# Kernel optimization log

Hardware: AMD Instinct MI355X
Metric: run time of the kernel (lower is better)

The kernel has to match this reference:

```python
import jax, jax.numpy as jnp
import numpy as np

E, D, H, T = 64, 512, 1024, 256  # num_experts, dim, hidden_dim, tokens


def setup_inputs() -> dict:
    key = jax.random.key(0)
    k1, k2, k3, k4 = jax.random.split(key, 4)
    x = jax.random.normal(k1, (T, D), dtype=jnp.float32)
    expert_idx = jax.random.randint(k2, (T,), 0, E, dtype=jnp.int64)
    # kaiming_uniform-ish init scale for the batched expert weights
    fc1_w = jax.random.normal(k3, (E, H, D), dtype=jnp.float32) * 0.02  # [E, hidden, dim]
    fc2_w = jax.random.normal(k4, (E, D, H), dtype=jnp.float32) * 0.02  # [E, dim, hidden]
    return {"x": x, "expert_idx": expert_idx, "fc1_w": fc1_w, "fc2_w": fc2_w}


def reference(x, expert_idx, fc1_w, fc2_w):
    # Gather full expert weight matrices per token (faithful to torch module),
    # then per-token matvec: out = silu(x @ W1^T) @ W2^T
    w1 = fc1_w[expert_idx]                      # [T, H, D]
    w2 = fc2_w[expert_idx]                      # [T, D, H]
    h = jax.nn.silu(jnp.einsum('td,thd->th', x, w1))  # [T, H]
    out = jnp.einsum('th,tdh->td', h, w2)             # [T, D]
    return out
```

## Files before the change

### kernel.cpp

```cpp
#include <hip/hip_runtime.h>
#include <math.h>

#define NE 64
#define ND 512
#define NH 1024
#define NT 256
#define NC 8


__device__ __forceinline__ int build_group(const int* __restrict__ idx, int e,
                                           int* tok_lds, int* wsum) {
    const int t = threadIdx.x, wave = t >> 6, lane = t & 63;
    const bool m = (idx[t] == e);
    const unsigned long long mask = __ballot(m);
    if (lane == 0) wsum[wave] = __popcll(mask);
    __syncthreads();
    int before = 0;
#pragma unroll
    for (int w = 0; w < 3; ++w) before += (w < wave) ? wsum[w] : 0;
    const int nt = wsum[0] + wsum[1] + wsum[2] + wsum[3];
    if (m) {
        int pos = before + __popcll(mask & ((1ull << lane) - 1ull));
        tok_lds[pos] = t;
    }
    __syncthreads();
    if (nt > 0 && t >= nt && t < nt + NC) tok_lds[t] = tok_lds[0];
    __syncthreads();
    return nt;
}

__device__ __forceinline__ float fused_reduce8_64(float v[NC], int lane) {
#pragma unroll
    for (int i = 0; i < 4; ++i) {
        float lo = v[i], hi = v[i + 4];
        float send = (lane & 1) ? lo : hi;
        float recv = __shfl_xor(send, 1);
        v[i] = ((lane & 1) ? hi : lo) + recv;
    }
#pragma unroll
    for (int i = 0; i < 2; ++i) {
        float lo = v[i], hi = v[i + 2];
        float send = (lane & 2) ? lo : hi;
        float recv = __shfl_xor(send, 2);
        v[i] = ((lane & 2) ? hi : lo) + recv;
    }
    {
        float lo = v[0], hi = v[1];
        float send = (lane & 4) ? lo : hi;
        float recv = __shfl_xor(send, 4);
        v[0] = ((lane & 4) ? hi : lo) + recv;
    }
    v[0] += __shfl_xor(v[0], 8);
    v[0] += __shfl_xor(v[0], 16);
    v[0] += __shfl_xor(v[0], 32);
    return v[0];
}

__device__ __forceinline__ float fused_reduce4_64(float v[4], int lane) {
#pragma unroll
    for (int i = 0; i < 2; ++i) {
        float lo = v[i], hi = v[i + 2];
        float send = (lane & 1) ? lo : hi;
        float recv = __shfl_xor(send, 1);
        v[i] = ((lane & 1) ? hi : lo) + recv;
    }
    {
        float lo = v[0], hi = v[1];
        float send = (lane & 2) ? lo : hi;
        float recv = __shfl_xor(send, 2);
        v[0] = ((lane & 2) ? hi : lo) + recv;
    }
    v[0] += __shfl_xor(v[0], 4);
    v[0] += __shfl_xor(v[0], 8);
    v[0] += __shfl_xor(v[0], 16);
    v[0] += __shfl_xor(v[0], 32);
    return v[0];
}

__global__ __launch_bounds__(256) void fc1_kernel(
    const float* __restrict__ x, const float* __restrict__ w1,
    const int* __restrict__ idx, float* __restrict__ h) {
    __shared__ int tok_lds[NT + NC];
    __shared__ int wsum[4];
    const int e  = blockIdx.x >> 5;
    const int ch = blockIdx.x & 31;
    const int tid = threadIdx.x, wave = tid >> 6, lane = tid & 63;
    const int nt = build_group(idx, e, tok_lds, wsum);
    if (nt == 0) return;
    const float* w1e = w1 + (size_t)e * NH * ND;
    const int jw = ch * 32 + wave * 8;

    for (int base = 0; base < nt; base += NC) {
        float4 xa[NC], xb[NC];
#pragma unroll
        for (int t = 0; t < NC; ++t) {
            const float* xr = x + (size_t)tok_lds[base + t] * ND;
            xa[t] = *(const float4*)(xr + lane * 4);
            xb[t] = *(const float4*)(xr + 256 + lane * 4);
        }
#pragma unroll 4
        for (int r = 0; r < 8; ++r) {
            const float* wr = w1e + (size_t)(jw + r) * ND;
            const float4 wa = *(const float4*)(wr + lane * 4);
            const float4 wb = *(const float4*)(wr + 256 + lane * 4);
            float acc[NC];
#pragma unroll
            for (int t = 0; t < NC; ++t) {
                acc[t] = wa.x * xa[t].x + wa.y * xa[t].y + wa.z * xa[t].z + wa.w * xa[t].w
                       + wb.x * xb[t].x + wb.y * xb[t].y + wb.z * xb[t].z + wb.w * xb[t].w;
            }
            float p = fused_reduce8_64(acc, lane);
            if (lane < NC) {
                int t = ((lane & 1) << 2) | (lane & 2) | ((lane >> 2) & 1);
                if (base + t < nt) {
                    int tk = tok_lds[base + t];
                    float s = p / (1.0f + __expf(-p));
                    h[(size_t)tk * NH + (jw + r)] = s;
                }
            }
        }
    }
}

__global__ __launch_bounds__(256) void fc2_kernel(
    const float* __restrict__ h, const float* __restrict__ w2,
    const int* __restrict__ idx, float* __restrict__ out) {
    __shared__ int tok_lds[NT + NC];
    __shared__ int wsum[4];
    const int e  = blockIdx.x >> 5;
    const int ch = blockIdx.x & 31;
    const int tid = threadIdx.x, wave = tid >> 6, lane = tid & 63;
    const int nt = build_group(idx, e, tok_lds, wsum);
    if (nt == 0) return;
    const float* w2e = w2 + (size_t)e * ND * NH;
    const int d0 = ch * 16 + wave * 4;

    for (int base = 0; base < nt; base += 4) {
        float4 hb0[4], hb1[4], hb2[4], hb3[4];
#pragma unroll
        for (int t = 0; t < 4; ++t) {
            const float* hr = h + (size_t)tok_lds[base + t] * NH;
            hb0[t] = *(const float4*)(hr + lane * 4);
            hb1[t] = *(const float4*)(hr + 256 + lane * 4);
            hb2[t] = *(const float4*)(hr + 512 + lane * 4);
            hb3[t] = *(const float4*)(hr + 768 + lane * 4);
        }
#pragma unroll
        for (int r = 0; r < 4; ++r) {
            const float* wr = w2e + (size_t)(d0 + r) * NH;
            const float4 w0 = *(const float4*)(wr + lane * 4);
            const float4 w1v = *(const float4*)(wr + 256 + lane * 4);
            const float4 w2v = *(const float4*)(wr + 512 + lane * 4);
            const float4 w3v = *(const float4*)(wr + 768 + lane * 4);
            float acc[4];
#pragma unroll
            for (int t = 0; t < 4; ++t) {
                acc[t] = w0.x * hb0[t].x + w0.y * hb0[t].y + w0.z * hb0[t].z + w0.w * hb0[t].w
                       + w1v.x * hb1[t].x + w1v.y * hb1[t].y + w1v.z * hb1[t].z + w1v.w * hb1[t].w
                       + w2v.x * hb2[t].x + w2v.y * hb2[t].y + w2v.z * hb2[t].z + w2v.w * hb2[t].w
                       + w3v.x * hb3[t].x + w3v.y * hb3[t].y + w3v.z * hb3[t].z + w3v.w * hb3[t].w;
            }
            float p = fused_reduce4_64(acc, lane);
            if (lane < 4) {
                int t = ((lane & 1) << 1) | ((lane >> 1) & 1);
                int slot = base + t;
                if (slot < nt) {
                    int tk = tok_lds[slot];
                    out[(size_t)tk * ND + (d0 + r)] = p;
                }
            }
        }
    }
}

extern "C" void kernel_launch(void* const* d_in, const int* in_sizes, int n_in,
                              void* d_out, int out_size, void* d_ws, size_t ws_size,
                              hipStream_t stream) {
    const float* x    = (const float*)d_in[0];
    const int*   eidx = (const int*)d_in[1];
    const float* fc1w = (const float*)d_in[2];
    const float* fc2w = (const float*)d_in[3];
    float* out = (float*)d_out;
    float* h   = (float*)d_ws;

    fc1_kernel<<<NE * 32, 256, 0, stream>>>(x, fc1w, eidx, h);
    fc2_kernel<<<NE * 32, 256, 0, stream>>>(h, fc2w, eidx, out);
}
```

Before: 60.26 us.

## Fuse fc1 and fc2 into one kernel with per-expert atomic barrier

Merges the two expert matvec kernels into one launch of 512 blocks, 8 per expert. Each block computes a larger slice of fc1, then waits on a per-expert atomic counter before doing its slice of fc2. This removes the second kernel launch and the inter-kernel gap, but adds a memset, a spin barrier, and reduces the number of in-flight waves that stream weights. The barrier relies on all blocks being co-resident.

```diff
diff --git a/kernel.cpp b/kernel.cpp
--- a/kernel.cpp
+++ b/kernel.cpp
@@ -77,96 +77,104 @@
     return v[0];
 }
 
-__global__ __launch_bounds__(256) void fc1_kernel(
+__global__ __launch_bounds__(256, 2) void moe_kernel(
     const float* __restrict__ x, const float* __restrict__ w1,
-    const int* __restrict__ idx, float* __restrict__ h) {
+    const float* __restrict__ w2, const int* __restrict__ idx,
+    float* __restrict__ h, int* __restrict__ done, float* __restrict__ out) {
     __shared__ int tok_lds[NT + NC];
     __shared__ int wsum[4];
-    const int e  = blockIdx.x >> 5;
-    const int ch = blockIdx.x & 31;
+    const int b = blockIdx.x;
+    const int e = b >> 3;
+    const int c = b & 7;
     const int tid = threadIdx.x, wave = tid >> 6, lane = tid & 63;
     const int nt = build_group(idx, e, tok_lds, wsum);
     if (nt == 0) return;
-    const float* w1e = w1 + (size_t)e * NH * ND;
-    const int jw = ch * 32 + wave * 8;
 
-    for (int base = 0; base < nt; base += NC) {
-        float4 xa[NC], xb[NC];
-#pragma unroll
-        for (int t = 0; t < NC; ++t) {
-            const float* xr = x + (size_t)tok_lds[base + t] * ND;
-            xa[t] = *(const float4*)(xr + lane * 4);
-            xb[t] = *(const float4*)(xr + 256 + lane * 4);
-        }
-#pragma unroll 4
-        for (int r = 0; r < 8; ++r) {
-            const float* wr = w1e + (size_t)(jw + r) * ND;
-            const float4 wa = *(const float4*)(wr + lane * 4);
-            const float4 wb = *(const float4*)(wr + 256 + lane * 4);
-            float acc[NC];
+    {
+        const float* w1e = w1 + (size_t)e * NH * ND;
+        const int jw = c * 128 + wave * 32;
+        for (int base = 0; base < nt; base += NC) {
+            float4 xa[NC], xb[NC];
 #pragma unroll
             for (int t = 0; t < NC; ++t) {
-                acc[t] = wa.x * xa[t].x + wa.y * xa[t].y + wa.z * xa[t].z + wa.w * xa[t].w
-                       + wb.x * xb[t].x + wb.y * xb[t].y + wb.z * xb[t].z + wb.w * xb[t].w;
+                const float* xr = x + (size_t)tok_lds[base + t] * ND;
+                xa[t] = *(const float4*)(xr + lane * 4);
+                xb[t] = *(const float4*)(xr + 256 + lane * 4);
             }
-            float p = fused_reduce8_64(acc, lane);
-            if (lane < NC) {
-                int t = ((lane & 1) << 2) | (lane & 2) | ((lane >> 2) & 1);
-                if (base + t < nt) {
-                    int tk = tok_lds[base + t];
-                    float s = p / (1.0f + __expf(-p));
-                    h[(size_t)tk * NH + (jw + r)] = s;
+#pragma unroll 4
+            for (int r = 0; r < 32; ++r) {
+                const float* wr = w1e + (size_t)(jw + r) * ND;
+                const float4 wa = *(const float4*)(wr + lane * 4);
+                const float4 wb = *(const float4*)(wr + 256 + lane * 4);
+                float acc[NC];
+#pragma unroll
+                for (int t = 0; t < NC; ++t) {
+                    acc[t] = wa.x * xa[t].x + wa.y * xa[t].y + wa.z * xa[t].z + wa.w * xa[t].w
+                           + wb.x * xb[t].x + wb.y * xb[t].y + wb.z * xb[t].z + wb.w * xb[t].w;
+                }
+                float p = fused_reduce8_64(acc, lane);
+                if (lane < NC) {
+                    int t = ((lane & 1) << 2) | (lane & 2) | ((lane >> 2) & 1);
+                    if (base + t < nt) {
+                        int tk = tok_lds[base + t];
+                        float s = p / (1.0f + __expf(-p));
+                        h[(size_t)tk * NH + (jw + r)] = s;
+                    }
                 }
             }
         }
     }
-}
 
-__global__ __launch_bounds__(256) void fc2_kernel(
-    const float* __restrict__ h, const float* __restrict__ w2,
-    const int* __restrict__ idx, float* __restrict__ out) {
-    __shared__ int tok_lds[NT + NC];
-    __shared__ int wsum[4];
-    const int e  = blockIdx.x >> 5;
-    const int ch = blockIdx.x & 31;
-    const int tid = threadIdx.x, wave = tid >> 6, lane = tid & 63;
-    const int nt = build_group(idx, e, tok_lds, wsum);
-    if (nt == 0) return;
-    const float* w2e = w2 + (size_t)e * ND * NH;
-    const int d0 = ch * 16 + wave * 4;
+    __syncthreads();
+    if (tid == 0) {
+        __hip_atomic_fetch_add(&done[e], 1, __ATOMIC_RELEASE,
+                               __HIP_MEMORY_SCOPE_AGENT);
+        int spins = 0;
+        while (__hip_atomic_load(&done[e], __ATOMIC_ACQUIRE,
+                                 __HIP_MEMORY_SCOPE_AGENT) < 8) {
+            __builtin_amdgcn_s_sleep(8);
+            if (++spins > (1 << 22)) break;
+        }
+    }
+    __syncthreads();
+    __threadfence();
 
-    for (int base = 0; base < nt; base += 4) {
-        float4 hb0[4], hb1[4], hb2[4], hb3[4];
-#pragma unroll
-        for (int t = 0; t < 4; ++t) {
-            const float* hr = h + (size_t)tok_lds[base + t] * NH;
-            hb0[t] = *(const float4*)(hr + lane * 4);
-            hb1[t] = *(const float4*)(hr + 256 + lane * 4);
-            hb2[t] = *(const float4*)(hr + 512 + lane * 4);
-            hb3[t] = *(const float4*)(hr + 768 + lane * 4);
-        }
-#pragma unroll
-        for (int r = 0; r < 4; ++r) {
-            const float* wr = w2e + (size_t)(d0 + r) * NH;
-            const float4 w0 = *(const float4*)(wr + lane * 4);
-            const float4 w1v = *(const float4*)(wr + 256 + lane * 4);
-            const float4 w2v = *(const float4*)(wr + 512 + lane * 4);
-            const float4 w3v = *(const float4*)(wr + 768 + lane * 4);
-            float acc[4];
+    {
+        const float* w2e = w2 + (size_t)e * ND * NH;
+        const int d0 = c * 64 + wave * 16;
+        for (int base = 0; base < nt; base += 4) {
+            float4 hb0[4], hb1[4], hb2[4], hb3[4];
 #pragma unroll
             for (int t = 0; t < 4; ++t) {
-                acc[t] = w0.x * hb0[t].x + w0.y * hb0[t].y + w0.z * hb0[t].z + w0.w * hb0[t].w
-                       + w1v.x * hb1[t].x + w1v.y * hb1[t].y + w1v.z * hb1[t].z + w1v.w * hb1[t].w
-                       + w2v.x * hb2[t].x + w2v.y * hb2[t].y + w2v.z * hb2[t].z + w2v.w * hb2[t].w
-                       + w3v.x * hb3[t].x + w3v.y * hb3[t].y + w3v.z * hb3[t].z + w3v.w * hb3[t].w;
+                const float* hr = h + (size_t)tok_lds[base + t] * NH;
+                hb0[t] = *(const float4*)(hr + lane * 4);
+                hb1[t] = *(const float4*)(hr + 256 + lane * 4);
+                hb2[t] = *(const float4*)(hr + 512 + lane * 4);
+                hb3[t] = *(const float4*)(hr + 768 + lane * 4);
             }
-            float p = fused_reduce4_64(acc, lane);
-            if (lane < 4) {
-                int t = ((lane & 1) << 1) | ((lane >> 1) & 1);
-                int slot = base + t;
-                if (slot < nt) {
-                    int tk = tok_lds[slot];
-                    out[(size_t)tk * ND + (d0 + r)] = p;
+#pragma unroll 4
+            for (int r = 0; r < 16; ++r) {
+                const float* wr = w2e + (size_t)(d0 + r) * NH;
+                const float4 w0 = *(const float4*)(wr + lane * 4);
+                const float4 w1v = *(const float4*)(wr + 256 + lane * 4);
+                const float4 w2v = *(const float4*)(wr + 512 + lane * 4);
+                const float4 w3v = *(const float4*)(wr + 768 + lane * 4);
+                float acc[4];
+#pragma unroll
+                for (int t = 0; t < 4; ++t) {
+                    acc[t] = w0.x * hb0[t].x + w0.y * hb0[t].y + w0.z * hb0[t].z + w0.w * hb0[t].w
+                           + w1v.x * hb1[t].x + w1v.y * hb1[t].y + w1v.z * hb1[t].z + w1v.w * hb1[t].w
+                           + w2v.x * hb2[t].x + w2v.y * hb2[t].y + w2v.z * hb2[t].z + w2v.w * hb2[t].w
+                           + w3v.x * hb3[t].x + w3v.y * hb3[t].y + w3v.z * hb3[t].z + w3v.w * hb3[t].w;
+                }
+                float p = fused_reduce4_64(acc, lane);
+                if (lane < 4) {
+                    int t = ((lane & 1) << 1) | ((lane >> 1) & 1);
+                    int slot = base + t;
+                    if (slot < nt) {
+                        int tk = tok_lds[slot];
+                        out[(size_t)tk * ND + (d0 + r)] = p;
+                    }
                 }
             }
         }
@@ -180,9 +188,10 @@
     const int*   eidx = (const int*)d_in[1];
     const float* fc1w = (const float*)d_in[2];
     const float* fc2w = (const float*)d_in[3];
-    float* out = (float*)d_out;
-    float* h   = (float*)d_ws;
+    float* out  = (float*)d_out;
+    int*   done = (int*)d_ws;
+    float* h    = (float*)((char*)d_ws + 256);
 
-    fc1_kernel<<<NE * 32, 256, 0, stream>>>(x, fc1w, eidx, h);
-    fc2_kernel<<<NE * 32, 256, 0, stream>>>(h, fc2w, eidx, out);
+    hipMemsetAsync(done, 0, 256, stream);
+    moe_kernel<<<512, 256, 0, stream>>>(x, fc1w, fc2w, eidx, h, done, out);
 }
```

After: 179.3 us. 2.98x slower.
